# Kernel tuning notes

Hardware: AMD Instinct MI355X
Metric: run time of the kernel (lower is better)

Reference implementation:

```python
import jax, jax.numpy as jnp
import numpy as np

B, T, N_EMBD = 1, 512, 768
N_HEAD, N_KV_HEAD = 12, 6
HEAD_DIM = N_EMBD // N_HEAD  # 64


def rms_norm(x, eps=1e-6):
    return x * jax.lax.rsqrt(jnp.mean(x * x, axis=-1, keepdims=True) + eps)


def apply_rotary_emb(x, cos, sin):
    # x: [B, T, H, D]; cos/sin: [T, D//2]
    d2 = x.shape[-1] // 2
    x1, x2 = x[..., :d2], x[..., d2:]
    c = cos[None, :, None, :]
    s = sin[None, :, None, :]
    return jnp.concatenate([x1 * c - x2 * s, x2 * c + x1 * s], axis=-1)


def tropical_dot_product(q, k):
    # q: [B,H,T,D], k: [B,H,S,D] -> max-plus score [B,H,T,S]
    return jnp.max(q[..., :, None, :] + k[..., None, :, :], axis=-1)


def setup_inputs() -> dict:
    key = jax.random.key(0)
    ks = jax.random.split(key, 5)
    x = jax.random.normal(ks[0], (B, T, N_EMBD), dtype=jnp.float32)
    # Real RoPE tables
    half = HEAD_DIM // 2
    inv_freq = 1.0 / (10000.0 ** (np.arange(0, half, dtype=np.float32) / half))
    t = np.arange(T, dtype=np.float32)
    freqs = np.outer(t, inv_freq)  # [T, D//2]
    cos = jnp.asarray(np.cos(freqs), dtype=jnp.float32)
    sin = jnp.asarray(np.sin(freqs), dtype=jnp.float32)
    std = 0.02
    Wq = std * jax.random.normal(ks[1], (N_EMBD, N_HEAD * HEAD_DIM), dtype=jnp.float32)
    Wk = std * jax.random.normal(ks[2], (N_EMBD, N_KV_HEAD * HEAD_DIM), dtype=jnp.float32)
    Wv = std * jax.random.normal(ks[3], (N_EMBD, N_KV_HEAD * HEAD_DIM), dtype=jnp.float32)
    Wproj = std * jax.random.normal(ks[4], (N_EMBD, N_EMBD), dtype=jnp.float32)
    return {"x": x, "cos": cos, "sin": sin, "Wq": Wq, "Wk": Wk, "Wv": Wv, "Wproj": Wproj}


def reference(x, cos, sin, Wq, Wk, Wv, Wproj):
    b, t, c = x.shape
    q = (x @ Wq).reshape(b, t, N_HEAD, HEAD_DIM)
    k = (x @ Wk).reshape(b, t, N_KV_HEAD, HEAD_DIM)
    v = (x @ Wv).reshape(b, t, N_KV_HEAD, HEAD_DIM)
    q = rms_norm(apply_rotary_emb(q, cos, sin))
    k = rms_norm(apply_rotary_emb(k, cos, sin))
    q = jnp.transpose(q, (0, 2, 1, 3))  # [B,H,T,D]
    k = jnp.transpose(k, (0, 2, 1, 3))  # [B,Hkv,T,D]
    v = jnp.transpose(v, (0, 2, 1, 3))
    n_rep = N_HEAD // N_KV_HEAD
    if n_rep > 1:
        k = jnp.repeat(k, n_rep, axis=1)
        v = jnp.repeat(v, n_rep, axis=1)
    scores = tropical_dot_product(q, k)  # [B,H,T,T]
    causal = jnp.tril(jnp.ones((t, t), dtype=jnp.bool_))
    scores = scores + jnp.where(causal, 0.0, -jnp.inf)
    attn = jax.nn.softmax(scores, axis=-1)
    y = jnp.einsum('bhqk,bhkd->bhqd', attn, v)
    y = jnp.transpose(y, (0, 2, 1, 3)).reshape(b, t, c)
    return y @ Wproj
```

## Files before the change

### kernel.cpp

```cpp
#include <hip/hip_runtime.h>
#include <hip/hip_bf16.h>
#include <math.h>

#define TT   512
#define CEMB 768
#define NH   12
#define NKV  6
#define HD   64
#define KVC  (NKV*HD)

typedef short short8 __attribute__((ext_vector_type(8)));
typedef float floatx4 __attribute__((ext_vector_type(4)));

__device__ __forceinline__ unsigned pack_bf16(float lo, float hi){
  __hip_bfloat162 h = __float22bfloat162_rn(make_float2(lo, hi));
  return *reinterpret_cast<unsigned*>(&h);
}
__device__ __forceinline__ unsigned short bf16_rn(float f){
  unsigned u = __float_as_uint(f);
  u += 0x7FFFu + ((u>>16)&1u);
  return (unsigned short)(u>>16);
}

__global__ void __launch_bounds__(256) gemm_qkv_mfma(
    const float* __restrict__ X,
    const float* __restrict__ Wq, const float* __restrict__ Wk, const float* __restrict__ Wv,
    const float* __restrict__ Wp,
    const float* __restrict__ cosb, const float* __restrict__ sinb,
    float* __restrict__ q, float* __restrict__ k, float* __restrict__ v,
    unsigned short* __restrict__ WpF){
  int bx = blockIdx.x;
  if (bx >= 192){
    int t0 = (bx-192)*256 + threadIdx.x;
    for(int g=0; g<8; ++g){
      int u  = g*9216 + t0;
      int kp = u / 192;
      int n4 = (u - kp*192)*4;
      int kk = kp*2;
      float4 w0 = *(const float4*)&Wp[(size_t)kk*CEMB + n4];
      float4 w1 = *(const float4*)&Wp[(size_t)(kk+1)*CEMB + n4];
      int ks = kk>>5, qq = (kk>>3)&3, j = kk&7;
      #pragma unroll
      for(int i=0;i<4;i++){
        int n = n4+i, ct = n>>4, r = n&15;
        *(unsigned*)&WpF[ (((size_t)(ct*24 + ks)*64 + qq*16 + r)<<3) + j ] =
          pack_bf16((&w0.x)[i], (&w1.x)[i]);
      }
    }
    return;
  }
  int mt = bx / 24, nt = bx % 24;
  const float* W; int ldb, bcol;
  if (nt < 12)      { W = Wq; ldb = CEMB; bcol = nt*64; }
  else if (nt < 18) { W = Wk; ldb = KVC;  bcol = (nt-12)*64; }
  else              { W = Wv; ldb = KVC;  bcol = (nt-18)*64; }

  __shared__ __align__(16) unsigned short Al[2][64][40];
  __shared__ __align__(16) unsigned short Bl[2][64][40];

  int tid = threadIdx.x;
  int am  = tid>>2,  akg = (tid&3)*8;
  int bkp = tid>>4,  bn4 = (tid&15)*4;
  int w = tid>>6, lane = tid&63, qq = lane>>4, r = lane&15;

  floatx4 acc[4];
  #pragma unroll
  for(int c=0;c<4;c++) acc[c] = (floatx4){0.f,0.f,0.f,0.f};

  const float* Ap = X + (size_t)(mt*64 + am)*CEMB + akg;
  const float* Bp = W + (size_t)(2*bkp)*ldb + bcol + bn4;

  float4 a0 = *(const float4*)(Ap);
  float4 a1 = *(const float4*)(Ap + 4);
  float4 b0 = *(const float4*)(Bp);
  float4 b1 = *(const float4*)(Bp + ldb);

  int buf = 0;
  for(int k0=0; k0<CEMB; k0+=32){
    unsigned p0 = pack_bf16(a0.x,a0.y), p1 = pack_bf16(a0.z,a0.w);
    unsigned p2 = pack_bf16(a1.x,a1.y), p3 = pack_bf16(a1.z,a1.w);
    *(uint4*)&Al[buf][am][akg] = make_uint4(p0,p1,p2,p3);
    #pragma unroll
    for(int i=0;i<4;i++)
      *(unsigned*)&Bl[buf][bn4+i][2*bkp] = pack_bf16((&b0.x)[i], (&b1.x)[i]);
    if (k0 + 32 < CEMB){
      a0 = *(const float4*)(Ap + k0+32);
      a1 = *(const float4*)(Ap + k0+36);
      b0 = *(const float4*)(Bp + (size_t)(k0+32)*ldb);
      b1 = *(const float4*)(Bp + (size_t)(k0+33)*ldb);
    }
    __syncthreads();
    short8 af = *(short8*)&Al[buf][w*16 + r][qq*8];
    #pragma unroll
    for(int c=0;c<4;c++){
      short8 bf = *(short8*)&Bl[buf][c*16 + r][qq*8];
      acc[c] = __builtin_amdgcn_mfma_f32_16x16x32_bf16(af, bf, acc[c], 0,0,0);
    }
    buf ^= 1;
  }

  #pragma unroll
  for(int reg=0; reg<4; ++reg){
    int t = mt*64 + w*16 + qq*4 + reg;
    if (nt < 18){
      float cs0 = cosb[t*32 + r],      sn0 = sinb[t*32 + r];
      float cs1 = cosb[t*32 + 16 + r], sn1 = sinb[t*32 + 16 + r];
      float x0 = acc[0][reg], x1 = acc[1][reg], x2 = acc[2][reg], x3 = acc[3][reg];
      float n0 = x0*cs0 - x2*sn0;
      float n1 = x1*cs1 - x3*sn1;
      float n2 = x2*cs0 + x0*sn0;
      float n3 = x3*cs1 + x1*sn1;
      float ss = n0*n0 + n1*n1 + n2*n2 + n3*n3;
      ss += __shfl_xor(ss,1); ss += __shfl_xor(ss,2);
      ss += __shfl_xor(ss,4); ss += __shfl_xor(ss,8);
      float sc = rsqrtf(ss*(1.0f/64.0f) + 1e-6f);
      float* dst = (nt < 12) ? (q + (size_t)t*CEMB + nt*64)
                             : (k + (size_t)t*KVC + (nt-12)*64);
      dst[r]    = n0*sc; dst[16+r] = n1*sc;
      dst[32+r] = n2*sc; dst[48+r] = n3*sc;
    } else {
      float* dst = v + (size_t)t*KVC + (nt-18)*64;
      dst[r]    = acc[0][reg]; dst[16+r] = acc[1][reg];
      dst[32+r] = acc[2][reg]; dst[48+r] = acc[3][reg];
    }
  }
}

__global__ void __launch_bounds__(256) attn_tile(const float* __restrict__ qn,
    const float* __restrict__ kn, const float* __restrict__ vr,
    float* __restrict__ part_acc, float2* __restrict__ part_ml){
  __shared__ float QPsh[64*68];
  __shared__ float Ksh[64*64];
  __shared__ float Vsh[64*64];

  int h   = blockIdx.y;
  int idx = blockIdx.x;
  int qt = 0, rem = idx;
  while (rem > qt){ rem -= (qt+1); ++qt; }
  int ct = rem;
  int t0 = ct*64;

  int kvh  = h >> 1;
  int w    = threadIdx.x >> 6;
  int lane = threadIdx.x & 63;
  int lg   = lane >> 4;
  int lc   = lane & 15;

  #pragma unroll
  for(int sub=0; sub<4; ++sub){
    int rr = w*16 + sub*4 + lg;
    int sw = ((lc ^ (rr>>2)) & 15)*4;
    *(float4*)&QPsh[rr*68 + lc*4] =
      *(const float4*)&qn[(size_t)(qt*64+rr)*CEMB + h*HD + lc*4];
    *(float4*)&Ksh[rr*64 + sw] =
      *(const float4*)&kn[(size_t)(t0+rr)*KVC + kvh*HD + lc*4];
    *(float4*)&Vsh[rr*64 + sw] =
      *(const float4*)&vr[(size_t)(t0+rr)*KVC + kvh*HD + lc*4];
  }
  __syncthreads();

  float s[4][4];
  #pragma unroll
  for(int r=0;r<4;r++)
    #pragma unroll
    for(int c=0;c<4;c++) s[r][c] = -INFINITY;

  #pragma unroll
  for(int dg=0; dg<16; ++dg){
    float4 k4[4], q4[4];
    int ksw = ((dg ^ lc)&15)*4;
    #pragma unroll
    for(int c=0;c<4;c++)
      k4[c] = *(const float4*)&Ksh[(lc*4+c)*64 + ksw];
    #pragma unroll
    for(int r=0;r<4;r++)
      q4[r] = *(const float4*)&QPsh[(w*16+lg*4+r)*68 + dg*4];
    #pragma unroll
    for(int r=0;r<4;r++)
      #pragma unroll
      for(int c=0;c<4;c++)
        s[r][c] = fmaxf(s[r][c],
                  fmaxf(fmaxf(q4[r].x + k4[c].x, q4[r].y + k4[c].y),
                        fmaxf(q4[r].z + k4[c].z, q4[r].w + k4[c].w)));
  }

  float mrow[4], lrow[4];
  #pragma unroll
  for(int r=0;r<4;r++){
    int i = qt*64 + w*16 + lg*4 + r;
    #pragma unroll
    for(int c=0;c<4;c++)
      if (t0 + lc*4 + c > i) s[r][c] = -INFINITY;
    float mt = fmaxf(fmaxf(s[r][0],s[r][1]), fmaxf(s[r][2],s[r][3]));
    mt = fmaxf(mt, __shfl_xor(mt,1));
    mt = fmaxf(mt, __shfl_xor(mt,2));
    mt = fmaxf(mt, __shfl_xor(mt,4));
    mt = fmaxf(mt, __shfl_xor(mt,8));
    float p0 = __expf(s[r][0]-mt), p1 = __expf(s[r][1]-mt);
    float p2 = __expf(s[r][2]-mt), p3 = __expf(s[r][3]-mt);
    float ps = p0+p1+p2+p3;
    ps += __shfl_xor(ps,1); ps += __shfl_xor(ps,2);
    ps += __shfl_xor(ps,4); ps += __shfl_xor(ps,8);
    mrow[r] = mt; lrow[r] = ps;
    *(float4*)&QPsh[(w*16+lg*4+r)*68 + lc*4] = make_float4(p0,p1,p2,p3);
  }
  __builtin_amdgcn_wave_barrier();

  float acc[4][4];
  #pragma unroll
  for(int r=0;r<4;r++)
    #pragma unroll
    for(int c=0;c<4;c++) acc[r][c] = 0.f;

  #pragma unroll
  for(int jg=0; jg<16; ++jg){
    float4 v4[4], p4[4];
    int vsw = ((lc ^ jg)&15)*4;
    #pragma unroll
    for(int jj=0;jj<4;jj++)
      v4[jj] = *(const float4*)&Vsh[(jg*4+jj)*64 + vsw];
    #pragma unroll
    for(int r=0;r<4;r++)
      p4[r] = *(const float4*)&QPsh[(w*16+lg*4+r)*68 + jg*4];
    #pragma unroll
    for(int r=0;r<4;r++)
      #pragma unroll
      for(int c=0;c<4;c++)
        acc[r][c] = fmaf(p4[r].x, (&v4[0].x)[c], fmaf(p4[r].y, (&v4[1].x)[c],
                    fmaf(p4[r].z, (&v4[2].x)[c], fmaf(p4[r].w, (&v4[3].x)[c], acc[r][c]))));
  }

  #pragma unroll
  for(int r=0;r<4;r++){
    int i = qt*64 + w*16 + lg*4 + r;
    int pidx = (h*TT + i)*8 + ct;
    *(float4*)&part_acc[(size_t)pidx*64 + lc*4] =
      make_float4(acc[r][0],acc[r][1],acc[r][2],acc[r][3]);
    if (lc == 0) part_ml[pidx] = make_float2(mrow[r], lrow[r]);
  }
}

__global__ void __launch_bounds__(256) attn_reduce(const float* __restrict__ part_acc,
    const float2* __restrict__ part_ml, unsigned short* __restrict__ yF){
  int wid  = (blockIdx.x * blockDim.x + threadIdx.x) >> 6;
  int lane = threadIdx.x & 63;
  int h = wid >> 9;
  int i = wid & 511;
  int nch = (i >> 6) + 1;
  int base = (h*TT + i)*8;

  float2 mls[8]; float acs[8];
  #pragma unroll
  for(int c=0;c<8;c++){
    mls[c] = part_ml[base + c];
    acs[c] = part_acc[(size_t)(base + c)*64 + lane];
  }

  float m = -INFINITY, l = 0.f, a = 0.f;
  #pragma unroll
  for(int c=0;c<8;c++){
    if (c < nch){
      float m_new = fmaxf(m, mls[c].x);
      float sa  = __expf(m - m_new);
      float sc_ = __expf(mls[c].x - m_new);
      l = l*sa + mls[c].y*sc_;
      a = a*sa + acs[c]*sc_;
      m = m_new;
    }
  }
  float val = a / l;
  int s = i>>4, rr = i&15;
  int ks = h*2 + (lane>>5), q2 = (lane>>3)&3, j = lane&7;
  yF[ (((size_t)(s*24 + ks)*64 + q2*16 + rr)<<3) + j ] = bf16_rn(val);
}

__global__ void __launch_bounds__(256) gemm_proj_mfma(
    const unsigned short* __restrict__ yF, const unsigned short* __restrict__ WpF,
    float* __restrict__ out){
  int bx = blockIdx.x;
  int mt = bx / 24, ntH = bx % 24;
  int tid = threadIdx.x, w = tid>>6, lane = tid&63, qq = lane>>4, r = lane&15;
  int s = mt*4 + w;

  const short8* Af = (const short8*)yF  + (size_t)s*24*64 + lane;
  const short8* Bf = (const short8*)WpF + lane;

  floatx4 acc[2];
  acc[0] = (floatx4){0.f,0.f,0.f,0.f};
  acc[1] = (floatx4){0.f,0.f,0.f,0.f};

  short8 ac_ = Af[0];
  short8 bc_[2];
  #pragma unroll
  for(int c=0;c<2;c++) bc_[c] = Bf[(size_t)((ntH*2+c)*24)*64];

  for(int ks=0; ks<24; ++ks){
    short8 an; short8 bn[2];
    if (ks < 23){
      an = Af[(size_t)(ks+1)*64];
      #pragma unroll
      for(int c=0;c<2;c++) bn[c] = Bf[(size_t)((ntH*2+c)*24 + ks+1)*64];
    }
    #pragma unroll
    for(int c=0;c<2;c++)
      acc[c] = __builtin_amdgcn_mfma_f32_16x16x32_bf16(ac_, bc_[c], acc[c], 0,0,0);
    if (ks < 23){
      ac_ = an;
      #pragma unroll
      for(int c=0;c<2;c++) bc_[c] = bn[c];
    }
  }

  #pragma unroll
  for(int reg=0; reg<4; ++reg){
    int t = mt*64 + w*16 + qq*4 + reg;
    float* dst = out + (size_t)t*CEMB + ntH*32;
    #pragma unroll
    for(int c=0;c<2;c++)
      dst[c*16 + r] = acc[c][reg];
  }
}

extern "C" void kernel_launch(void* const* d_in, const int* in_sizes, int n_in,
                              void* d_out, int out_size, void* d_ws, size_t ws_size,
                              hipStream_t stream){
  const float* x    = (const float*)d_in[0];
  const float* cosb = (const float*)d_in[1];
  const float* sinb = (const float*)d_in[2];
  const float* Wq   = (const float*)d_in[3];
  const float* Wk   = (const float*)d_in[4];
  const float* Wv   = (const float*)d_in[5];
  const float* Wp   = (const float*)d_in[6];
  float* out = (float*)d_out;

  float* ws        = (float*)d_ws;
  float* q_raw     = ws;
  float* k_raw     = q_raw + (size_t)TT*CEMB;
  float* v_raw     = k_raw + (size_t)TT*KVC;
  float* part_acc  = v_raw + (size_t)TT*KVC;
  float2* part_ml  = (float2*)(part_acc + (size_t)NH*TT*8*64);
  unsigned short* WpF = (unsigned short*)(part_ml + (size_t)NH*TT*8);
  unsigned short* yF  = WpF + (size_t)48*24*64*8;

  gemm_qkv_mfma <<<dim3(228),   256, 0, stream>>>(x, Wq, Wk, Wv, Wp, cosb, sinb,
                                                  q_raw, k_raw, v_raw, WpF);
  attn_tile     <<<dim3(36,NH), 256, 0, stream>>>(q_raw, k_raw, v_raw, part_acc, part_ml);
  attn_reduce   <<<dim3(NH*TT/4), 256, 0, stream>>>(part_acc, part_ml, yF);
  gemm_proj_mfma<<<dim3(192),   256, 0, stream>>>(yF, WpF, out);
}
```

Before: 116.3 us.

## Fuse four kernels into one cooperative persistent kernel with grid syncs

Combines the QKV GEMM, attention tile, reduce and projection kernels into a single cooperative kernel. Blocks loop over work units, separated by grid.sync barriers, and the stages share LDS through a union. The goal is to remove three kernel launch gaps and inter-kernel drains. The cost is grid-wide barrier overhead, reduced parallelism in stages that have fewer units than the grid (e.g. 228 or 192 units on a 512-block grid), and possible register pressure from launch_bounds(256,2). The old four-kernel path is kept as a fallback if the cooperative launch fails.

Result: slower. 283.5 us (+143.8%).

```diff
diff --git a/kernel.cpp b/kernel.cpp
--- a/kernel.cpp
+++ b/kernel.cpp
@@ -1,6 +1,9 @@
 #include <hip/hip_runtime.h>
+#include <hip/hip_cooperative_groups.h>
 #include <hip/hip_bf16.h>
 #include <math.h>
+
+namespace cg = cooperative_groups;
 
 #define TT   512
 #define CEMB 768
@@ -22,43 +25,39 @@
   return (unsigned short)(u>>16);
 }
 
-__global__ void __launch_bounds__(256) gemm_qkv_mfma(
+
+__device__ __forceinline__ void body_wp_pack(int u, int tid,
+    const float* __restrict__ Wp, unsigned short* __restrict__ WpF){
+  int t0 = u*256 + tid;
+  for(int g=0; g<8; ++g){
+    int uu = g*9216 + t0;
+    int kp = uu / 192;
+    int n4 = (uu - kp*192)*4;
+    int kk = kp*2;
+    float4 w0 = *(const float4*)&Wp[(size_t)kk*CEMB + n4];
+    float4 w1 = *(const float4*)&Wp[(size_t)(kk+1)*CEMB + n4];
+    int ks = kk>>5, qq = (kk>>3)&3, j = kk&7;
+    #pragma unroll
+    for(int i=0;i<4;i++){
+      int n = n4+i, ct = n>>4, r = n&15;
+      *(unsigned*)&WpF[ (((size_t)(ct*24 + ks)*64 + qq*16 + r)<<3) + j ] =
+        pack_bf16((&w0.x)[i], (&w1.x)[i]);
+    }
+  }
+}
+
+__device__ __forceinline__ void body_qkv_tile(int u, int tid,
+    unsigned short (*Al)[64][40], unsigned short (*Bl)[64][40],
     const float* __restrict__ X,
     const float* __restrict__ Wq, const float* __restrict__ Wk, const float* __restrict__ Wv,
-    const float* __restrict__ Wp,
     const float* __restrict__ cosb, const float* __restrict__ sinb,
-    float* __restrict__ q, float* __restrict__ k, float* __restrict__ v,
-    unsigned short* __restrict__ WpF){
-  int bx = blockIdx.x;
-  if (bx >= 192){
-    int t0 = (bx-192)*256 + threadIdx.x;
-    for(int g=0; g<8; ++g){
-      int u  = g*9216 + t0;
-      int kp = u / 192;
-      int n4 = (u - kp*192)*4;
-      int kk = kp*2;
-      float4 w0 = *(const float4*)&Wp[(size_t)kk*CEMB + n4];
-      float4 w1 = *(const float4*)&Wp[(size_t)(kk+1)*CEMB + n4];
-      int ks = kk>>5, qq = (kk>>3)&3, j = kk&7;
-      #pragma unroll
-      for(int i=0;i<4;i++){
-        int n = n4+i, ct = n>>4, r = n&15;
-        *(unsigned*)&WpF[ (((size_t)(ct*24 + ks)*64 + qq*16 + r)<<3) + j ] =
-          pack_bf16((&w0.x)[i], (&w1.x)[i]);
-      }
-    }
-    return;
-  }
-  int mt = bx / 24, nt = bx % 24;
+    float* __restrict__ q, float* __restrict__ k, float* __restrict__ v){
+  int mt = u / 24, nt = u % 24;
   const float* W; int ldb, bcol;
   if (nt < 12)      { W = Wq; ldb = CEMB; bcol = nt*64; }
   else if (nt < 18) { W = Wk; ldb = KVC;  bcol = (nt-12)*64; }
   else              { W = Wv; ldb = KVC;  bcol = (nt-18)*64; }
 
-  __shared__ __align__(16) unsigned short Al[2][64][40];
-  __shared__ __align__(16) unsigned short Bl[2][64][40];
-
-  int tid = threadIdx.x;
   int am  = tid>>2,  akg = (tid&3)*8;
   int bkp = tid>>4,  bn4 = (tid&15)*4;
   int w = tid>>6, lane = tid&63, qq = lane>>4, r = lane&15;
@@ -126,23 +125,21 @@
   }
 }
 
-__global__ void __launch_bounds__(256) attn_tile(const float* __restrict__ qn,
-    const float* __restrict__ kn, const float* __restrict__ vr,
+__device__ __forceinline__ void body_attn_tile(int u, int tid,
+    float* QPsh, float* Ksh, float* Vsh,
+    const float* __restrict__ qn, const float* __restrict__ kn,
+    const float* __restrict__ vr,
     float* __restrict__ part_acc, float2* __restrict__ part_ml){
-  __shared__ float QPsh[64*68];
-  __shared__ float Ksh[64*64];
-  __shared__ float Vsh[64*64];
-
-  int h   = blockIdx.y;
-  int idx = blockIdx.x;
+  int h   = u / 36;
+  int idx = u % 36;
   int qt = 0, rem = idx;
   while (rem > qt){ rem -= (qt+1); ++qt; }
   int ct = rem;
   int t0 = ct*64;
 
   int kvh  = h >> 1;
-  int w    = threadIdx.x >> 6;
-  int lane = threadIdx.x & 63;
+  int w    = tid >> 6;
+  int lane = tid & 63;
   int lg   = lane >> 4;
   int lc   = lane & 15;
 
@@ -240,10 +237,9 @@
   }
 }
 
-__global__ void __launch_bounds__(256) attn_reduce(const float* __restrict__ part_acc,
-    const float2* __restrict__ part_ml, unsigned short* __restrict__ yF){
-  int wid  = (blockIdx.x * blockDim.x + threadIdx.x) >> 6;
-  int lane = threadIdx.x & 63;
+__device__ __forceinline__ void body_reduce(int wid, int lane,
+    const float* __restrict__ part_acc, const float2* __restrict__ part_ml,
+    unsigned short* __restrict__ yF){
   int h = wid >> 9;
   int i = wid & 511;
   int nch = (i >> 6) + 1;
@@ -274,12 +270,11 @@
   yF[ (((size_t)(s*24 + ks)*64 + q2*16 + rr)<<3) + j ] = bf16_rn(val);
 }
 
-__global__ void __launch_bounds__(256) gemm_proj_mfma(
+__device__ __forceinline__ void body_proj(int u, int tid,
     const unsigned short* __restrict__ yF, const unsigned short* __restrict__ WpF,
     float* __restrict__ out){
-  int bx = blockIdx.x;
-  int mt = bx / 24, ntH = bx % 24;
-  int tid = threadIdx.x, w = tid>>6, lane = tid&63, qq = lane>>4, r = lane&15;
+  int mt = u / 24, ntH = u % 24;
+  int w = tid>>6, lane = tid&63, qq = lane>>4, r = lane&15;
   int s = mt*4 + w;
 
   const short8* Af = (const short8*)yF  + (size_t)s*24*64 + lane;
@@ -319,6 +314,78 @@
     for(int c=0;c<2;c++)
       dst[c*16 + r] = acc[c][reg];
   }
+}
+
+struct SmemGemm { unsigned short Al[2][64][40]; unsigned short Bl[2][64][40]; };
+struct SmemAttn { float QP[64*68]; float K[64*64]; float V[64*64]; };
+union Smem { SmemGemm g; SmemAttn a; };
+
+__global__ void __launch_bounds__(256,2) mega(
+    const float* __restrict__ X,
+    const float* __restrict__ cosb, const float* __restrict__ sinb,
+    const float* __restrict__ Wq, const float* __restrict__ Wk,
+    const float* __restrict__ Wv, const float* __restrict__ Wp,
+    float* __restrict__ q, float* __restrict__ k, float* __restrict__ v,
+    float* __restrict__ part_acc, float2* __restrict__ part_ml,
+    unsigned short* __restrict__ WpF, unsigned short* __restrict__ yF,
+    float* __restrict__ out){
+  __shared__ Smem sm;
+  cg::grid_group grid = cg::this_grid();
+  const int tid = threadIdx.x;
+  const int w = tid>>6, lane = tid&63;
+
+  for (int u = blockIdx.x; u < 228; u += gridDim.x){
+    if (u >= 192){ body_wp_pack(u-192, tid, Wp, WpF); continue; }
+    __syncthreads();
+    body_qkv_tile(u, tid, sm.g.Al, sm.g.Bl, X, Wq, Wk, Wv, cosb, sinb, q, k, v);
+  }
+  grid.sync();
+
+  for (int u = blockIdx.x; u < 432; u += gridDim.x){
+    __syncthreads();
+    body_attn_tile(u, tid, sm.a.QP, sm.a.K, sm.a.V, q, k, v, part_acc, part_ml);
+  }
+  grid.sync();
+
+  for (int u = blockIdx.x; u < 1536; u += gridDim.x)
+    body_reduce(u*4 + w, lane, part_acc, part_ml, yF);
+  grid.sync();
+
+  for (int u = blockIdx.x; u < 192; u += gridDim.x)
+    body_proj(u, tid, yF, WpF, out);
+}
+
+__global__ void __launch_bounds__(256) gemm_qkv_mfma(
+    const float* __restrict__ X,
+    const float* __restrict__ Wq, const float* __restrict__ Wk, const float* __restrict__ Wv,
+    const float* __restrict__ Wp,
+    const float* __restrict__ cosb, const float* __restrict__ sinb,
+    float* __restrict__ q, float* __restrict__ k, float* __restrict__ v,
+    unsigned short* __restrict__ WpF){
+  __shared__ SmemGemm sg;
+  int bx = blockIdx.x;
+  if (bx >= 192){ body_wp_pack(bx-192, threadIdx.x, Wp, WpF); return; }
+  body_qkv_tile(bx, threadIdx.x, sg.Al, sg.Bl, X, Wq, Wk, Wv, cosb, sinb, q, k, v);
+}
+
+__global__ void __launch_bounds__(256) attn_tile_k(const float* __restrict__ qn,
+    const float* __restrict__ kn, const float* __restrict__ vr,
+    float* __restrict__ part_acc, float2* __restrict__ part_ml){
+  __shared__ SmemAttn sa;
+  int u = blockIdx.y*36 + blockIdx.x;
+  body_attn_tile(u, threadIdx.x, sa.QP, sa.K, sa.V, qn, kn, vr, part_acc, part_ml);
+}
+
+__global__ void __launch_bounds__(256) attn_reduce_k(const float* __restrict__ part_acc,
+    const float2* __restrict__ part_ml, unsigned short* __restrict__ yF){
+  int wid  = (blockIdx.x * blockDim.x + threadIdx.x) >> 6;
+  body_reduce(wid, threadIdx.x & 63, part_acc, part_ml, yF);
+}
+
+__global__ void __launch_bounds__(256) gemm_proj_mfma(
+    const unsigned short* __restrict__ yF, const unsigned short* __restrict__ WpF,
+    float* __restrict__ out){
+  body_proj(blockIdx.x, threadIdx.x, yF, WpF, out);
 }
 
 extern "C" void kernel_launch(void* const* d_in, const int* in_sizes, int n_in,
@@ -342,9 +409,28 @@
   unsigned short* WpF = (unsigned short*)(part_ml + (size_t)NH*TT*8);
   unsigned short* yF  = WpF + (size_t)48*24*64*8;
 
-  gemm_qkv_mfma <<<dim3(228),   256, 0, stream>>>(x, Wq, Wk, Wv, Wp, cosb, sinb,
-                                                  q_raw, k_raw, v_raw, WpF);
-  attn_tile     <<<dim3(36,NH), 256, 0, stream>>>(q_raw, k_raw, v_raw, part_acc, part_ml);
-  attn_reduce   <<<dim3(NH*TT/4), 256, 0, stream>>>(part_acc, part_ml, yF);
-  gemm_proj_mfma<<<dim3(192),   256, 0, stream>>>(yF, WpF, out);
-}
+  int occ = 0;
+  hipError_t qe = hipOccupancyMaxActiveBlocksPerMultiprocessor(
+                    &occ, (const void*)mega, 256, 0);
+  hipError_t le = hipErrorUnknown;
+  if (qe == hipSuccess && occ >= 1){
+    int grid = occ >= 2 ? 512 : 256;
+    void* kargs[] = {
+      (void*)&x, (void*)&cosb, (void*)&sinb,
+      (void*)&Wq, (void*)&Wk, (void*)&Wv, (void*)&Wp,
+      (void*)&q_raw, (void*)&k_raw, (void*)&v_raw,
+      (void*)&part_acc, (void*)&part_ml,
+      (void*)&WpF, (void*)&yF, (void*)&out
+    };
+    le = hipLaunchCooperativeKernel((void*)mega, dim3(grid), dim3(256),
+                                    kargs, 0, stream);
+  }
+  if (le != hipSuccess){
+    gemm_qkv_mfma <<<dim3(228),   256, 0, stream>>>(x, Wq, Wk, Wv, Wp, cosb, sinb,
+                                                    q_raw, k_raw, v_raw, WpF);
+    attn_tile_k   <<<dim3(36,NH), 256, 0, stream>>>(q_raw, k_raw, v_raw,
+                                                    part_acc, part_ml);
+    attn_reduce_k <<<dim3(NH*TT/4), 256, 0, stream>>>(part_acc, part_ml, yF);
+    gemm_proj_mfma<<<dim3(192),   256, 0, stream>>>(yF, WpF, out);
+  }
+}
```

## Use bf16 MFMA for P·V in attention tile and load A fragments directly

Applied to the files above, without the earlier changes.

The attention tile kernel now stores softmax probabilities as bf16 in shared memory and V transposed as bf16. It computes P·V with 16x16x32 bf16 MFMA instructions instead of scalar fp32 FMAs. The QKV GEMM also skips the shared-memory staging of the X tile: each lane loads its own A fragment straight from global memory and packs it into registers. This cuts FMA work and LDS traffic, at the cost of bf16 rounding of P and V, uncoalesced global A loads, and a scattered column-wise partial-accumulator store.

Result: slower. 120.4 us (+3.5%).

```diff
diff --git a/kernel.cpp b/kernel.cpp
--- a/kernel.cpp
+++ b/kernel.cpp
@@ -55,11 +55,9 @@
   else if (nt < 18) { W = Wk; ldb = KVC;  bcol = (nt-12)*64; }
   else              { W = Wv; ldb = KVC;  bcol = (nt-18)*64; }
 
-  __shared__ __align__(16) unsigned short Al[2][64][40];
   __shared__ __align__(16) unsigned short Bl[2][64][40];
 
   int tid = threadIdx.x;
-  int am  = tid>>2,  akg = (tid&3)*8;
   int bkp = tid>>4,  bn4 = (tid&15)*4;
   int w = tid>>6, lane = tid&63, qq = lane>>4, r = lane&15;
 
@@ -67,30 +65,29 @@
   #pragma unroll
   for(int c=0;c<4;c++) acc[c] = (floatx4){0.f,0.f,0.f,0.f};
 
-  const float* Ap = X + (size_t)(mt*64 + am)*CEMB + akg;
+  const float* Ax = X + (size_t)(mt*64 + w*16 + r)*CEMB + qq*8;
   const float* Bp = W + (size_t)(2*bkp)*ldb + bcol + bn4;
 
-  float4 a0 = *(const float4*)(Ap);
-  float4 a1 = *(const float4*)(Ap + 4);
+  float4 a0 = *(const float4*)(Ax);
+  float4 a1 = *(const float4*)(Ax + 4);
   float4 b0 = *(const float4*)(Bp);
   float4 b1 = *(const float4*)(Bp + ldb);
 
   int buf = 0;
   for(int k0=0; k0<CEMB; k0+=32){
-    unsigned p0 = pack_bf16(a0.x,a0.y), p1 = pack_bf16(a0.z,a0.w);
-    unsigned p2 = pack_bf16(a1.x,a1.y), p3 = pack_bf16(a1.z,a1.w);
-    *(uint4*)&Al[buf][am][akg] = make_uint4(p0,p1,p2,p3);
+    uint4 afu = make_uint4(pack_bf16(a0.x,a0.y), pack_bf16(a0.z,a0.w),
+                           pack_bf16(a1.x,a1.y), pack_bf16(a1.z,a1.w));
+    short8 af; __builtin_memcpy(&af, &afu, 16);
     #pragma unroll
     for(int i=0;i<4;i++)
       *(unsigned*)&Bl[buf][bn4+i][2*bkp] = pack_bf16((&b0.x)[i], (&b1.x)[i]);
     if (k0 + 32 < CEMB){
-      a0 = *(const float4*)(Ap + k0+32);
-      a1 = *(const float4*)(Ap + k0+36);
+      a0 = *(const float4*)(Ax + k0+32);
+      a1 = *(const float4*)(Ax + k0+36);
       b0 = *(const float4*)(Bp + (size_t)(k0+32)*ldb);
       b1 = *(const float4*)(Bp + (size_t)(k0+33)*ldb);
     }
     __syncthreads();
-    short8 af = *(short8*)&Al[buf][w*16 + r][qq*8];
     #pragma unroll
     for(int c=0;c<4;c++){
       short8 bf = *(short8*)&Bl[buf][c*16 + r][qq*8];
@@ -129,9 +126,10 @@
 __global__ void __launch_bounds__(256) attn_tile(const float* __restrict__ qn,
     const float* __restrict__ kn, const float* __restrict__ vr,
     float* __restrict__ part_acc, float2* __restrict__ part_ml){
-  __shared__ float QPsh[64*68];
+  __shared__ float Qsh[64*68];
   __shared__ float Ksh[64*64];
-  __shared__ float Vsh[64*64];
+  __shared__ __align__(16) unsigned short Pl[64][72];
+  __shared__ __align__(16) unsigned short VshT[64][72];
 
   int h   = blockIdx.y;
   int idx = blockIdx.x;
@@ -150,12 +148,15 @@
   for(int sub=0; sub<4; ++sub){
     int rr = w*16 + sub*4 + lg;
     int sw = ((lc ^ (rr>>2)) & 15)*4;
-    *(float4*)&QPsh[rr*68 + lc*4] =
+    *(float4*)&Qsh[rr*68 + lc*4] =
       *(const float4*)&qn[(size_t)(qt*64+rr)*CEMB + h*HD + lc*4];
     *(float4*)&Ksh[rr*64 + sw] =
       *(const float4*)&kn[(size_t)(t0+rr)*KVC + kvh*HD + lc*4];
-    *(float4*)&Vsh[rr*64 + sw] =
-      *(const float4*)&vr[(size_t)(t0+rr)*KVC + kvh*HD + lc*4];
+    float4 vf = *(const float4*)&vr[(size_t)(t0+rr)*KVC + kvh*HD + lc*4];
+    VshT[lc*4+0][rr] = bf16_rn(vf.x);
+    VshT[lc*4+1][rr] = bf16_rn(vf.y);
+    VshT[lc*4+2][rr] = bf16_rn(vf.z);
+    VshT[lc*4+3][rr] = bf16_rn(vf.w);
   }
   __syncthreads();
 
@@ -174,7 +175,7 @@
       k4[c] = *(const float4*)&Ksh[(lc*4+c)*64 + ksw];
     #pragma unroll
     for(int r=0;r<4;r++)
-      q4[r] = *(const float4*)&QPsh[(w*16+lg*4+r)*68 + dg*4];
+      q4[r] = *(const float4*)&Qsh[(w*16+lg*4+r)*68 + dg*4];
     #pragma unroll
     for(int r=0;r<4;r++)
       #pragma unroll
@@ -184,7 +185,6 @@
                         fmaxf(q4[r].z + k4[c].z, q4[r].w + k4[c].w)));
   }
 
-  float mrow[4], lrow[4];
   #pragma unroll
   for(int r=0;r<4;r++){
     int i = qt*64 + w*16 + lg*4 + r;
@@ -201,42 +201,34 @@
     float ps = p0+p1+p2+p3;
     ps += __shfl_xor(ps,1); ps += __shfl_xor(ps,2);
     ps += __shfl_xor(ps,4); ps += __shfl_xor(ps,8);
-    mrow[r] = mt; lrow[r] = ps;
-    *(float4*)&QPsh[(w*16+lg*4+r)*68 + lc*4] = make_float4(p0,p1,p2,p3);
+    *(uint2*)&Pl[w*16+lg*4+r][lc*4] =
+      make_uint2(pack_bf16(p0,p1), pack_bf16(p2,p3));
+    if (lc == 0)
+      part_ml[(h*TT + i)*8 + ct] = make_float2(mt, ps);
   }
   __builtin_amdgcn_wave_barrier();
 
-  float acc[4][4];
-  #pragma unroll
-  for(int r=0;r<4;r++)
-    #pragma unroll
-    for(int c=0;c<4;c++) acc[r][c] = 0.f;
-
-  #pragma unroll
-  for(int jg=0; jg<16; ++jg){
-    float4 v4[4], p4[4];
-    int vsw = ((lc ^ jg)&15)*4;
-    #pragma unroll
-    for(int jj=0;jj<4;jj++)
-      v4[jj] = *(const float4*)&Vsh[(jg*4+jj)*64 + vsw];
-    #pragma unroll
-    for(int r=0;r<4;r++)
-      p4[r] = *(const float4*)&QPsh[(w*16+lg*4+r)*68 + jg*4];
-    #pragma unroll
-    for(int r=0;r<4;r++)
-      #pragma unroll
-      for(int c=0;c<4;c++)
-        acc[r][c] = fmaf(p4[r].x, (&v4[0].x)[c], fmaf(p4[r].y, (&v4[1].x)[c],
-                    fmaf(p4[r].z, (&v4[2].x)[c], fmaf(p4[r].w, (&v4[3].x)[c], acc[r][c]))));
-  }
-
-  #pragma unroll
-  for(int r=0;r<4;r++){
-    int i = qt*64 + w*16 + lg*4 + r;
+  floatx4 macc[4];
+  #pragma unroll
+  for(int c=0;c<4;c++) macc[c] = (floatx4){0.f,0.f,0.f,0.f};
+
+  short8 af1 = *(short8*)&Pl[w*16 + lc][lg*8];
+  short8 af2 = *(short8*)&Pl[w*16 + lc][32 + lg*8];
+  #pragma unroll
+  for(int c=0;c<4;c++){
+    short8 bf1 = *(short8*)&VshT[c*16 + lc][lg*8];
+    short8 bf2 = *(short8*)&VshT[c*16 + lc][32 + lg*8];
+    macc[c] = __builtin_amdgcn_mfma_f32_16x16x32_bf16(af1, bf1, macc[c], 0,0,0);
+    macc[c] = __builtin_amdgcn_mfma_f32_16x16x32_bf16(af2, bf2, macc[c], 0,0,0);
+  }
+
+  #pragma unroll
+  for(int reg=0; reg<4; ++reg){
+    int i = qt*64 + w*16 + lg*4 + reg;
     int pidx = (h*TT + i)*8 + ct;
-    *(float4*)&part_acc[(size_t)pidx*64 + lc*4] =
-      make_float4(acc[r][0],acc[r][1],acc[r][2],acc[r][3]);
-    if (lc == 0) part_ml[pidx] = make_float2(mrow[r], lrow[r]);
+    #pragma unroll
+    for(int c=0;c<4;c++)
+      part_acc[(size_t)pidx*64 + c*16 + lc] = macc[c][reg];
   }
 }
 
```
